# Performance work log

Measured on AMD Instinct MI355X. Metric: run time of the kernel, lower is better.

The kernel has to match this reference:

```python
import jax, jax.numpy as jnp
import numpy as np

VOCAB = 50000
PAD_ID = 1
N = 2048
SRC_L = 400


def setup_inputs() -> dict:
    key = jax.random.key(0)
    k1, k2, k3, k4, k5 = jax.random.split(key, 5)
    # probability-like inputs (pointer-generator produces softmax outputs)
    p_gen = jax.nn.softmax(jax.random.normal(k1, (N, VOCAB), dtype=jnp.float32), axis=-1)
    p_copy = jax.nn.softmax(jax.random.normal(k2, (N, SRC_L), dtype=jnp.float32), axis=-1)
    p_switch = jax.random.uniform(k3, (N,), dtype=jnp.float32)
    tgt = jax.random.randint(k4, (N,), 0, VOCAB)
    src = jax.random.randint(k5, (N, SRC_L), 0, VOCAB)
    return {"p_gen": p_gen, "p_copy": p_copy, "p_switch": p_switch, "tgt": tgt, "src": src}


def reference(p_gen, p_copy, p_switch, tgt, src):
    n, vocab = p_gen.shape
    sw = p_switch[:, None]  # [n,1]
    # generation part: p_gen * (1 - p_switch)
    gen_scores = p_gen * (1.0 - sw)
    # copy part: scatter_add p_copy into vocab-sized tensor along src indices
    rows = jnp.arange(n)[:, None]  # [n,1] broadcast with src [n,src_l]
    copy_scores = jnp.zeros((n, vocab), dtype=p_gen.dtype).at[rows, src].add(p_copy)
    # src.max() < vocab_size here, so c_vocab == vocab and the p_switch scale
    # applies to the whole copy distribution (matches torch code in this case)
    scores = copy_scores * sw + gen_scores  # [n, vocab]
    pred = jnp.argmax(scores, axis=1)
    eps = 1e-12
    non_padding = (tgt != PAD_ID).astype(scores.dtype)
    target_scores = jnp.take_along_axis(scores, tgt[:, None], axis=1)[:, 0]
    loss = -jnp.sum(jnp.log(target_scores + eps) * non_padding) / n
    return loss, pred
```

## Files before the change

### kernel.cpp

```cpp
#include <hip/hip_runtime.h>
#include <math.h>

#define NROWS  2048
#define VOCAB  50000
#define SRC_L  400
#define PAD_ID 1
#define NBM    1568
#define HSZ    1024
#define QCAP   64

__global__ __launch_bounds__(256) void pg_row_kernel(
    const float* __restrict__ p_gen,
    const float* __restrict__ p_copy,
    const float* __restrict__ p_switch,
    const int*   __restrict__ tgt,
    const int*   __restrict__ src,
    float* __restrict__ out,
    float* __restrict__ row_loss)
{
    const int row = blockIdx.x;
    const int tid = threadIdx.x;

    const float sw  = p_switch[row];
    const float osw = 1.0f - sw;
    const float* __restrict__ g = p_gen + (size_t)row * VOCAB;
    const int tv = tgt[row];

    __shared__ int      s_src[SRC_L];
    __shared__ float    s_pc [SRC_L];
    __shared__ unsigned s_bm [NBM];
    __shared__ int      s_key[HSZ];
    __shared__ float    s_val[HSZ];
    __shared__ int      s_qs [QCAP];
    __shared__ int      s_qv [QCAP];
    __shared__ int      s_qn;
    __shared__ float    s_gtv;

    for (int j = tid; j < SRC_L; j += 256) {
        s_src[j] = src[(size_t)row * SRC_L + j];
        s_pc [j] = p_copy[(size_t)row * SRC_L + j];
    }
    for (int i = tid; i < NBM; i += 256) s_bm[i] = 0u;
    for (int i = tid; i < HSZ; i += 256) s_key[i] = -1;
    if (tid == 0) s_qn = 0;
    __syncthreads();

    for (int j = tid; j < SRC_L; j += 256) {
        const int   v = s_src[j];
        const float p = s_pc [j];
        atomicOr(&s_bm[v >> 5], 1u << (v & 31));
        unsigned s = (((unsigned)v) * 2654435761u) >> 22;
        while (true) {
            const int old = atomicCAS(&s_key[s], -1, v);
            if (old == -1) { s_val[s] = p; break; }
            if (old == v) {
                const int qi = atomicAdd(&s_qn, 1);
                if (qi < QCAP) { s_qs[qi] = (int)s; s_qv[qi] = v; }
                break;
            }
            s = (s + 1) & (HSZ - 1);
        }
    }
    __syncthreads();

    if (tid < 64) {
        int qn = s_qn; if (qn > QCAP) qn = QCAP;
        const int lane = tid;
        for (int q = 0; q < qn; ++q) {
            const int slot = s_qs[q];
            const int v    = s_qv[q];
            float S = 0.0f;
            #pragma unroll
            for (int r = 0; r < 7; ++r) {
                const int k  = (r << 6) + lane;
                const int kk = (k < SRC_L) ? k : 0;
                const bool m = (k < SRC_L) && (s_src[kk] == v);
                const float pk = s_pc[kk];
                unsigned long long mask = __ballot(m);
                while (mask) {
                    const int l = __ffsll((long long)mask) - 1;
                    S = __fadd_rn(S, __shfl(pk, l));
                    mask &= mask - 1;
                }
            }
            if (lane == 0) s_val[slot] = S;
        }
    }
    __syncthreads();

    float bestv = -1.0f;
    int   besti = 0x7fffffff;

    const float4* __restrict__ g4 = (const float4*)g;
    for (int t = tid; t < VOCAB / 4; t += 256) {
        const float4 vv = g4[t];
        const int b = t << 2;
        const unsigned m4 = (s_bm[b >> 5] >> (b & 31)) & 0xFu;

        #define PG_ELT(i, comp)                                                 \
        {                                                                       \
            const float a = __fmul_rn(comp, osw);                               \
            if (a > bestv) { bestv = a; besti = b + (i); }                      \
            if (m4 & (1u << (i))) {                                             \
                const int v = b + (i);                                          \
                unsigned s = (((unsigned)v) * 2654435761u) >> 22;               \
                while (s_key[s] != v) s = (s + 1) & (HSZ - 1);                  \
                const float cand = __fadd_rn(__fmul_rn(sw, s_val[s]),           \
                                             __fmul_rn(osw, comp));             \
                if (cand > bestv) { bestv = cand; besti = v; }                  \
            }                                                                   \
        }
        PG_ELT(0, vv.x)
        PG_ELT(1, vv.y)
        PG_ELT(2, vv.z)
        PG_ELT(3, vv.w)
        #undef PG_ELT

        if (tv >= b && tv < b + 4) {
            float gt = vv.x;
            if      (tv == b + 1) gt = vv.y;
            else if (tv == b + 2) gt = vv.z;
            else if (tv == b + 3) gt = vv.w;
            s_gtv = gt;
        }
    }

    float tsum = 0.0f;
    for (int k = tid; k < SRC_L; k += 256)
        if (s_src[k] == tv) tsum += s_pc[k];

    for (int off = 32; off > 0; off >>= 1) {
        const float ov = __shfl_down(bestv, off);
        const int   oi = __shfl_down(besti, off);
        if (ov > bestv || (ov == bestv && oi < besti)) { bestv = ov; besti = oi; }
        tsum += __shfl_down(tsum, off);
    }

    __shared__ float wv[4];
    __shared__ int   wi[4];
    __shared__ float wsum[4];
    const int wave = tid >> 6;
    if ((tid & 63) == 0) { wv[wave] = bestv; wi[wave] = besti; wsum[wave] = tsum; }
    __syncthreads();

    if (tid == 0) {
        for (int w = 1; w < 4; ++w) {
            if (wv[w] > bestv || (wv[w] == bestv && wi[w] < besti)) {
                bestv = wv[w]; besti = wi[w];
            }
            tsum += wsum[w];
        }
        out[1 + row] = (float)besti;

        const float ts = __fadd_rn(__fmul_rn(sw, tsum), __fmul_rn(osw, s_gtv));
        row_loss[row] = (tv != PAD_ID) ? logf(ts + 1e-12f) : 0.0f;
    }
}

__global__ __launch_bounds__(256) void pg_loss_kernel(
    const float* __restrict__ row_loss,
    float* __restrict__ out)
{
    float s = 0.0f;
    for (int i = threadIdx.x; i < NROWS; i += 256) s += row_loss[i];
    for (int off = 32; off > 0; off >>= 1) s += __shfl_down(s, off);

    __shared__ float wsum[4];
    if ((threadIdx.x & 63) == 0) wsum[threadIdx.x >> 6] = s;
    __syncthreads();
    if (threadIdx.x == 0) {
        const float t = wsum[0] + wsum[1] + wsum[2] + wsum[3];
        out[0] = -t / (float)NROWS;
    }
}

extern "C" void kernel_launch(void* const* d_in, const int* in_sizes, int n_in,
                              void* d_out, int out_size, void* d_ws, size_t ws_size,
                              hipStream_t stream) {
    const float* p_gen    = (const float*)d_in[0];
    const float* p_copy   = (const float*)d_in[1];
    const float* p_switch = (const float*)d_in[2];
    const int*   tgt      = (const int*)d_in[3];
    const int*   src      = (const int*)d_in[4];

    float* out      = (float*)d_out;
    float* row_loss = (float*)d_ws;

    pg_row_kernel<<<NROWS, 256, 0, stream>>>(p_gen, p_copy, p_switch, tgt, src,
                                             out, row_loss);
    pg_loss_kernel<<<1, 256, 0, stream>>>(row_loss, out);
}
```

Before: 85.81 us.

## Prefetch p_gen tiles before hash build and fuse loss reduction via last-block counter

Issues the first four float4 loads of each p_gen row into registers before the shared-memory hash table is built, so global memory latency overlaps the setup phase. The separate loss-reduction kernel is removed; instead each block atomically bumps a workspace counter and the last block to finish sums row losses, saving one launch. The duplicate queue capacity is also doubled. Costs are extra register pressure from the prefetch buffers and reliance on a counter that is never reset, handled with a modulo check.

```diff
diff --git a/kernel.cpp b/kernel.cpp
--- a/kernel.cpp
+++ b/kernel.cpp
@@ -3,11 +3,13 @@
 
 #define NROWS  2048
 #define VOCAB  50000
+#define NQ     (VOCAB / 4)
 #define SRC_L  400
 #define PAD_ID 1
 #define NBM    1568
 #define HSZ    1024
-#define QCAP   64
+#define QCAP   128
+#define PF     4
 
 __global__ __launch_bounds__(256) void pg_row_kernel(
     const float* __restrict__ p_gen,
@@ -16,15 +18,13 @@
     const int*   __restrict__ tgt,
     const int*   __restrict__ src,
     float* __restrict__ out,
-    float* __restrict__ row_loss)
+    float* __restrict__ row_loss,
+    unsigned* __restrict__ counter)
 {
     const int row = blockIdx.x;
     const int tid = threadIdx.x;
-
-    const float sw  = p_switch[row];
-    const float osw = 1.0f - sw;
-    const float* __restrict__ g = p_gen + (size_t)row * VOCAB;
-    const int tv = tgt[row];
+    const float*  __restrict__ g  = p_gen + (size_t)row * VOCAB;
+    const float4* __restrict__ g4 = (const float4*)g;
 
     __shared__ int      s_src[SRC_L];
     __shared__ float    s_pc [SRC_L];
@@ -35,14 +35,33 @@
     __shared__ int      s_qv [QCAP];
     __shared__ int      s_qn;
     __shared__ float    s_gtv;
-
-    for (int j = tid; j < SRC_L; j += 256) {
-        s_src[j] = src[(size_t)row * SRC_L + j];
-        s_pc [j] = p_copy[(size_t)row * SRC_L + j];
-    }
+    __shared__ int      s_last;
+    __shared__ float    wv[4];
+    __shared__ int      wi[4];
+    __shared__ float    wsum[4];
+
+    const int  base = row * SRC_L;
+    const int  j1ok = (tid + 256 < SRC_L);
+    const int   rs0 = src[base + tid];
+    const float rp0 = p_copy[base + tid];
+    int rs1 = 0; float rp1 = 0.0f;
+    if (j1ok) { rs1 = src[base + tid + 256]; rp1 = p_copy[base + tid + 256]; }
+
+    float4 pfv[PF];
+    #pragma unroll
+    for (int k = 0; k < PF; ++k) pfv[k] = g4[tid + (k << 8)];
+
+    const float sw   = p_switch[row];
+    const float osw  = 1.0f - sw;
+    const int   tv   = tgt[row];
+    const int   t_tv = tv >> 2;
+
     for (int i = tid; i < NBM; i += 256) s_bm[i] = 0u;
     for (int i = tid; i < HSZ; i += 256) s_key[i] = -1;
     if (tid == 0) s_qn = 0;
+
+    s_src[tid] = rs0; s_pc[tid] = rp0;
+    if (j1ok) { s_src[tid + 256] = rs1; s_pc[tid + 256] = rp1; }
     __syncthreads();
 
     for (int j = tid; j < SRC_L; j += 256) {
@@ -91,39 +110,45 @@
     float bestv = -1.0f;
     int   besti = 0x7fffffff;
 
-    const float4* __restrict__ g4 = (const float4*)g;
-    for (int t = tid; t < VOCAB / 4; t += 256) {
-        const float4 vv = g4[t];
-        const int b = t << 2;
-        const unsigned m4 = (s_bm[b >> 5] >> (b & 31)) & 0xFu;
-
-        #define PG_ELT(i, comp)                                                 \
-        {                                                                       \
-            const float a = __fmul_rn(comp, osw);                               \
-            if (a > bestv) { bestv = a; besti = b + (i); }                      \
-            if (m4 & (1u << (i))) {                                             \
-                const int v = b + (i);                                          \
-                unsigned s = (((unsigned)v) * 2654435761u) >> 22;               \
-                while (s_key[s] != v) s = (s + 1) & (HSZ - 1);                  \
-                const float cand = __fadd_rn(__fmul_rn(sw, s_val[s]),           \
-                                             __fmul_rn(osw, comp));             \
-                if (cand > bestv) { bestv = cand; besti = v; }                  \
-            }                                                                   \
-        }
-        PG_ELT(0, vv.x)
-        PG_ELT(1, vv.y)
-        PG_ELT(2, vv.z)
-        PG_ELT(3, vv.w)
-        #undef PG_ELT
-
-        if (tv >= b && tv < b + 4) {
-            float gt = vv.x;
-            if      (tv == b + 1) gt = vv.y;
-            else if (tv == b + 2) gt = vv.z;
-            else if (tv == b + 3) gt = vv.w;
-            s_gtv = gt;
-        }
-    }
+    #define PG_ELT(b, i, comp)                                                  \
+    {                                                                           \
+        const float a = __fmul_rn(comp, osw);                                   \
+        if (a > bestv) { bestv = a; besti = (b) + (i); }                        \
+        if (m4 & (1u << (i))) {                                                 \
+            const int v = (b) + (i);                                            \
+            unsigned hs = (((unsigned)v) * 2654435761u) >> 22;                  \
+            while (s_key[hs] != v) hs = (hs + 1) & (HSZ - 1);                   \
+            const float cand = __fadd_rn(__fmul_rn(sw, s_val[hs]),              \
+                                         __fmul_rn(osw, comp));                 \
+            if (cand > bestv) { bestv = cand; besti = v; }                      \
+        }                                                                       \
+    }
+
+    #define PG_QUAD(t, vv)                                                      \
+    {                                                                           \
+        const int b = (t) << 2;                                                 \
+        const unsigned m4 = (s_bm[b >> 5] >> (b & 31)) & 0xFu;                  \
+        PG_ELT(b, 0, (vv).x)                                                    \
+        PG_ELT(b, 1, (vv).y)                                                    \
+        PG_ELT(b, 2, (vv).z)                                                    \
+        PG_ELT(b, 3, (vv).w)                                                    \
+        if ((t) == t_tv) {                                                      \
+            float gt = (vv).x;                                                  \
+            if      (tv == b + 1) gt = (vv).y;                                  \
+            else if (tv == b + 2) gt = (vv).z;                                  \
+            else if (tv == b + 3) gt = (vv).w;                                  \
+            s_gtv = gt;                                                         \
+        }                                                                       \
+    }
+
+    #pragma unroll
+    for (int k = 0; k < PF; ++k) { const int t = tid + (k << 8); PG_QUAD(t, pfv[k]) }
+    for (int t = tid + (PF << 8); t < NQ; t += 256) {
+        const float4 vvq = g4[t];
+        PG_QUAD(t, vvq)
+    }
+    #undef PG_QUAD
+    #undef PG_ELT
 
     float tsum = 0.0f;
     for (int k = tid; k < SRC_L; k += 256)
@@ -136,9 +161,6 @@
         tsum += __shfl_down(tsum, off);
     }
 
-    __shared__ float wv[4];
-    __shared__ int   wi[4];
-    __shared__ float wsum[4];
     const int wave = tid >> 6;
     if ((tid & 63) == 0) { wv[wave] = bestv; wi[wave] = besti; wsum[wave] = tsum; }
     __syncthreads();
@@ -153,24 +175,26 @@
         out[1 + row] = (float)besti;
 
         const float ts = __fadd_rn(__fmul_rn(sw, tsum), __fmul_rn(osw, s_gtv));
-        row_loss[row] = (tv != PAD_ID) ? logf(ts + 1e-12f) : 0.0f;
-    }
-}
-
-__global__ __launch_bounds__(256) void pg_loss_kernel(
-    const float* __restrict__ row_loss,
-    float* __restrict__ out)
-{
-    float s = 0.0f;
-    for (int i = threadIdx.x; i < NROWS; i += 256) s += row_loss[i];
-    for (int off = 32; off > 0; off >>= 1) s += __shfl_down(s, off);
-
-    __shared__ float wsum[4];
-    if ((threadIdx.x & 63) == 0) wsum[threadIdx.x >> 6] = s;
-    __syncthreads();
-    if (threadIdx.x == 0) {
-        const float t = wsum[0] + wsum[1] + wsum[2] + wsum[3];
-        out[0] = -t / (float)NROWS;
+        const float contrib = (tv != PAD_ID) ? logf(ts + 1e-12f) : 0.0f;
+        __hip_atomic_store(&row_loss[row], contrib,
+                           __ATOMIC_RELEASE, __HIP_MEMORY_SCOPE_AGENT);
+        const unsigned old = __hip_atomic_fetch_add(counter, 1u,
+                           __ATOMIC_ACQ_REL, __HIP_MEMORY_SCOPE_AGENT);
+        s_last = ((old & (NROWS - 1)) == (NROWS - 1));
+    }
+    __syncthreads();
+
+    if (s_last) {
+        __threadfence();
+        float s = 0.0f;
+        for (int i = tid; i < NROWS; i += 256)
+            s += __hip_atomic_load(&row_loss[i],
+                                   __ATOMIC_RELAXED, __HIP_MEMORY_SCOPE_AGENT);
+        for (int off = 32; off > 0; off >>= 1) s += __shfl_down(s, off);
+        if ((tid & 63) == 0) wsum[tid >> 6] = s;
+        __syncthreads();
+        if (tid == 0)
+            out[0] = -(wsum[0] + wsum[1] + wsum[2] + wsum[3]) / (float)NROWS;
     }
 }
 
@@ -183,10 +207,10 @@
     const int*   tgt      = (const int*)d_in[3];
     const int*   src      = (const int*)d_in[4];
 
-    float* out      = (float*)d_out;
-    float* row_loss = (float*)d_ws;
+    float*    out      = (float*)d_out;
+    float*    row_loss = (float*)d_ws;
+    unsigned* counter  = (unsigned*)((char*)d_ws + NROWS * sizeof(float));
 
     pg_row_kernel<<<NROWS, 256, 0, stream>>>(p_gen, p_copy, p_switch, tgt, src,
-                                             out, row_loss);
-    pg_loss_kernel<<<1, 256, 0, stream>>>(row_loss, out);
+                                             out, row_loss, counter);
 }
```

New measurement: 203.8 us. +137.5%, slower.
